# Optimization experiments

Measured on AMD Instinct MI355X. Metric: run time of the kernel, lower is better.

The kernel has to match this reference:

```python
import jax, jax.numpy as jnp
import numpy as np

TMP = 1.0  # temperature from init

def setup_inputs() -> dict:
    key = jax.random.key(0)
    k1, k2, k3 = jax.random.split(key, 3)
    B, D, C = 8192, 1024, 4096
    x = jax.random.normal(k1, (B, D), dtype=jnp.float32)
    mod = jax.random.normal(k2, (B, D), dtype=jnp.float32)
    W = jax.random.normal(k3, (C, D), dtype=jnp.float32) * 0.02  # cls.weight
    return {"x": x, "mod": mod, "W": W}

def reference(x, mod, W):
    # att = softmax(mod / tmp, axis=1) + 1, shape (B, D)
    att = jax.nn.softmax(mod / TMP, axis=1) + 1.0
    # result[b, c] = sum_d W[c, d] * att[b, d] * x[b, d]
    # == (att * x) @ W.T  -- collapses the repeat + per-sample matvec loop
    return jnp.einsum('bd,cd->bc', att * x, W)
```

## Files before the change

kernel.cpp:

```cpp
#include <hip/hip_runtime.h>
#include <hip/hip_bf16.h>
#include <cstdint>
#include <cstddef>

typedef __bf16 bf16_t;
typedef __bf16 bf16x8 __attribute__((ext_vector_type(8)));
typedef __bf16 bf16x4 __attribute__((ext_vector_type(4)));
typedef float  f32x4  __attribute__((ext_vector_type(4)));

#define KDIM 1024
#define NT   16

__global__ void att_scale_kernel(const float* __restrict__ x,
                                 const float* __restrict__ mod,
                                 bf16_t* __restrict__ a, int D) {
  const int b = blockIdx.x;
  const int t = threadIdx.x;
  const size_t row = (size_t)b * D;

  float4 mv = ((const float4*)(mod + row))[t];
  float mx = fmaxf(fmaxf(mv.x, mv.y), fmaxf(mv.z, mv.w));
#pragma unroll
  for (int o = 32; o > 0; o >>= 1) mx = fmaxf(mx, __shfl_xor(mx, o));

  __shared__ float redmax[4];
  __shared__ float redsum[4];
  const int wave = t >> 6, lane = t & 63;
  if (lane == 0) redmax[wave] = mx;
  __syncthreads();
  mx = fmaxf(fmaxf(redmax[0], redmax[1]), fmaxf(redmax[2], redmax[3]));

  float4 e;
  e.x = __expf(mv.x - mx); e.y = __expf(mv.y - mx);
  e.z = __expf(mv.z - mx); e.w = __expf(mv.w - mx);
  float s = (e.x + e.y) + (e.z + e.w);
#pragma unroll
  for (int o = 32; o > 0; o >>= 1) s += __shfl_xor(s, o);
  if (lane == 0) redsum[wave] = s;
  __syncthreads();
  s = (redsum[0] + redsum[1]) + (redsum[2] + redsum[3]);

  const float inv = 1.0f / s;
  float4 xv = ((const float4*)(x + row))[t];
  bf16x4 o4;
  o4[0] = (bf16_t)((e.x * inv + 1.0f) * xv.x);
  o4[1] = (bf16_t)((e.y * inv + 1.0f) * xv.y);
  o4[2] = (bf16_t)((e.z * inv + 1.0f) * xv.z);
  o4[3] = (bf16_t)((e.w * inv + 1.0f) * xv.w);
  *((bf16x4*)(a + row) + t) = o4;
}

__global__ void cast_w_kernel(const float* __restrict__ W,
                              bf16_t* __restrict__ Wb) {
  const size_t i = ((size_t)blockIdx.x * blockDim.x + threadIdx.x) * 8;
  float4 u = *(const float4*)(W + i);
  float4 v = *(const float4*)(W + i + 4);
  bf16x8 o;
  o[0] = (bf16_t)u.x; o[1] = (bf16_t)u.y; o[2] = (bf16_t)u.z; o[3] = (bf16_t)u.w;
  o[4] = (bf16_t)v.x; o[5] = (bf16_t)v.y; o[6] = (bf16_t)v.z; o[7] = (bf16_t)v.w;
  *(bf16x8*)(Wb + i) = o;
}

__global__ __launch_bounds__(512, 2) void gemm256_kernel(
    const bf16_t* __restrict__ A, const bf16_t* __restrict__ B,
    float* __restrict__ C, int M, int N) {
  __shared__ __align__(16) bf16_t lds[2 * 32768];

  const int tid  = threadIdx.x;
  const int wave = tid >> 6;
  const int lane = tid & 63;
  const int quad = lane >> 4;
  const int l16  = lane & 15;
  const int wm   = wave >> 2;
  const int wn   = wave & 3;

  const int nwg = gridDim.x;
  int flat = blockIdx.x;
  flat = (flat & 7) * (nwg >> 3) + (flat >> 3);
  const int ntiles = N >> 8;
  const int m0 = (flat / ntiles) << 8;
  const int n0 = (flat % ntiles) << 8;

  const int trow = tid >> 3;
  const int colg = (tid & 7) ^ (trow & 7);
  const bf16_t* aSrc = A + (size_t)(m0 + trow) * KDIM + colg * 8;
  const bf16_t* bSrc = B + (size_t)(n0 + trow) * KDIM + colg * 8;
  const int ldsW = wave * 512;

#define GLDS(src_, dst_) __builtin_amdgcn_global_load_lds( \
      (const __attribute__((address_space(1))) void*)(src_), \
      (__attribute__((address_space(3))) void*)(dst_), 16, 0, 0)

#define ISSUE_A(h, u_) do { \
      const bf16_t* s_ = aSrc + (size_t)((h) * 128) * KDIM + (u_) * 64; \
      bf16_t* d_ = lds + ((u_) & 1) * 32768 + (h) * 8192 + ldsW; \
      GLDS(s_, d_); \
      GLDS(s_ + (size_t)64 * KDIM, d_ + 4096); \
    } while (0)

#define ISSUE_B(h, u_) do { \
      const bf16_t* s_ = bSrc + (size_t)((h) * 128) * KDIM + (u_) * 64; \
      bf16_t* d_ = lds + ((u_) & 1) * 32768 + 16384 + (h) * 8192 + ldsW; \
      GLDS(s_, d_); \
      GLDS(s_ + (size_t)64 * KDIM, d_ + 4096); \
    } while (0)

  ISSUE_A(0, 0); ISSUE_A(1, 0);
  ISSUE_B(0, 0); ISSUE_B(1, 0);
  ISSUE_B(0, 1); ISSUE_B(1, 1);

  f32x4 acc[8][4];
#pragma unroll
  for (int i = 0; i < 8; ++i)
#pragma unroll
    for (int j = 0; j < 4; ++j) acc[i][j] = (f32x4){0.f, 0.f, 0.f, 0.f};

  const int aBase = (wm * 128 + l16) * 64;
  const int bBase = (wn * 64 + l16) * 64;
  const int c0 = ((quad)     ^ (l16 & 7)) * 8;
  const int c1 = ((4 + quad) ^ (l16 & 7)) * 8;

  asm volatile("s_waitcnt vmcnt(4)" ::: "memory");
  __builtin_amdgcn_s_barrier();

  bf16x8 bfr[4][2];

#define PHASE(q_, ISSUE_STMT, WAIT_STMT) do { \
      bf16x8 af[2][2]; \
      _Pragma("unroll") \
      for (int i = 0; i < 2; ++i) { \
        af[i][0] = *(const bf16x8*)(At + aBase + ((q_) * 32 + i * 16) * 64 + c0); \
        af[i][1] = *(const bf16x8*)(At + aBase + ((q_) * 32 + i * 16) * 64 + c1); \
      } \
      ISSUE_STMT; \
      asm volatile("" ::: "memory"); \
      __builtin_amdgcn_s_barrier(); \
      asm volatile("s_waitcnt lgkmcnt(0)" ::: "memory"); \
      __builtin_amdgcn_s_setprio(1); \
      _Pragma("unroll") \
      for (int i = 0; i < 2; ++i) \
        _Pragma("unroll") \
        for (int j = 0; j < 4; ++j) { \
          acc[(q_) * 2 + i][j] = __builtin_amdgcn_mfma_f32_16x16x32_bf16( \
              af[i][0], bfr[j][0], acc[(q_) * 2 + i][j], 0, 0, 0); \
          acc[(q_) * 2 + i][j] = __builtin_amdgcn_mfma_f32_16x16x32_bf16( \
              af[i][1], bfr[j][1], acc[(q_) * 2 + i][j], 0, 0, 0); \
        } \
      __builtin_amdgcn_s_setprio(0); \
      WAIT_STMT; \
      asm volatile("" ::: "memory"); \
      __builtin_amdgcn_s_barrier(); \
    } while (0)

#pragma unroll 1
  for (int u = 0; u < NT; ++u) {
    const bf16_t* At = lds + (u & 1) * 32768;
    const bf16_t* Bt = At + 16384;

#pragma unroll
    for (int j = 0; j < 4; ++j) {
      bfr[j][0] = *(const bf16x8*)(Bt + bBase + j * 16 * 64 + c0);
      bfr[j][1] = *(const bf16x8*)(Bt + bBase + j * 16 * 64 + c1);
    }
    PHASE(0, if (u + 1 < NT) ISSUE_A(0, u + 1), (void)0);
    PHASE(1, if (u + 1 < NT) ISSUE_A(1, u + 1), (void)0);
    PHASE(2, if (u + 2 < NT) ISSUE_B(0, u + 2), (void)0);
    PHASE(3, if (u + 2 < NT) ISSUE_B(1, u + 2),
          if (u < NT - 2) { asm volatile("s_waitcnt vmcnt(4)" ::: "memory"); }
          else            { asm volatile("s_waitcnt vmcnt(0)" ::: "memory"); });
  }

#pragma unroll
  for (int ri = 0; ri < 8; ++ri) {
    const int mg = m0 + wm * 128 + ri * 16 + quad * 4;
#pragma unroll
    for (int j = 0; j < 4; ++j) {
      const int ng = n0 + wn * 64 + j * 16 + l16;
#pragma unroll
      for (int r = 0; r < 4; ++r)
        C[(size_t)(mg + r) * N + ng] = acc[ri][j][r];
    }
  }
}

extern "C" void kernel_launch(void* const* d_in, const int* in_sizes, int n_in,
                              void* d_out, int out_size, void* d_ws, size_t ws_size,
                              hipStream_t stream) {
  const float* x   = (const float*)d_in[0];
  const float* mod = (const float*)d_in[1];
  const float* W   = (const float*)d_in[2];
  float* out = (float*)d_out;

  const int D = 1024;
  const int Bn = in_sizes[0] / D;
  const int Cn = in_sizes[2] / D;

  bf16_t* a  = (bf16_t*)d_ws;
  bf16_t* Wb = (bf16_t*)((char*)d_ws + (size_t)Bn * D * sizeof(bf16_t));

  att_scale_kernel<<<Bn, 256, 0, stream>>>(x, mod, a, D);
  cast_w_kernel<<<((size_t)Cn * D) / (256 * 8), 256, 0, stream>>>(W, Wb);

  const int nwg = (Bn / 256) * (Cn / 256);
  gemm256_kernel<<<nwg, 512, 0, stream>>>(a, Wb, out, Bn, Cn);
}
```

Measured before the change: 257.0 us.

## Fuse prep kernels and make each GEMM block process two M tiles continuously

Merges the softmax-scale and W-cast kernels into one launch. Each GEMM workgroup now computes two consecutive 256-row M tiles against the same N tile, running one continuous 32-step pipeline that flushes and resets the accumulators halfway. This removes a kernel launch, halves the GEMM grid so each block covers more work, and keeps the prefetch pipeline running across the tile boundary. The cost is half as many workgroups, which on a 256-CU device may lower occupancy and leave load imbalanced, plus a mid-loop store burst.

Result: slower. 272.9 us (+6.2%).

```diff
diff --git a/kernel.cpp b/kernel.cpp
--- a/kernel.cpp
+++ b/kernel.cpp
@@ -10,10 +10,25 @@
 
 #define KDIM 1024
 #define NT   16
-
-__global__ void att_scale_kernel(const float* __restrict__ x,
-                                 const float* __restrict__ mod,
-                                 bf16_t* __restrict__ a, int D) {
+#define NTT  32
+
+__global__ void prep_kernel(const float* __restrict__ x,
+                            const float* __restrict__ mod,
+                            const float* __restrict__ W,
+                            bf16_t* __restrict__ a,
+                            bf16_t* __restrict__ Wb,
+                            int D, int Bn) {
+  if ((int)blockIdx.x >= Bn) {
+    const size_t i = (((size_t)blockIdx.x - Bn) * blockDim.x + threadIdx.x) * 8;
+    float4 u = *(const float4*)(W + i);
+    float4 v = *(const float4*)(W + i + 4);
+    bf16x8 o;
+    o[0] = (bf16_t)u.x; o[1] = (bf16_t)u.y; o[2] = (bf16_t)u.z; o[3] = (bf16_t)u.w;
+    o[4] = (bf16_t)v.x; o[5] = (bf16_t)v.y; o[6] = (bf16_t)v.z; o[7] = (bf16_t)v.w;
+    *(bf16x8*)(Wb + i) = o;
+    return;
+  }
+
   const int b = blockIdx.x;
   const int t = threadIdx.x;
   const size_t row = (size_t)b * D;
@@ -50,17 +65,6 @@
   *((bf16x4*)(a + row) + t) = o4;
 }
 
-__global__ void cast_w_kernel(const float* __restrict__ W,
-                              bf16_t* __restrict__ Wb) {
-  const size_t i = ((size_t)blockIdx.x * blockDim.x + threadIdx.x) * 8;
-  float4 u = *(const float4*)(W + i);
-  float4 v = *(const float4*)(W + i + 4);
-  bf16x8 o;
-  o[0] = (bf16_t)u.x; o[1] = (bf16_t)u.y; o[2] = (bf16_t)u.z; o[3] = (bf16_t)u.w;
-  o[4] = (bf16_t)v.x; o[5] = (bf16_t)v.y; o[6] = (bf16_t)v.z; o[7] = (bf16_t)v.w;
-  *(bf16x8*)(Wb + i) = o;
-}
-
 __global__ __launch_bounds__(512, 2) void gemm256_kernel(
     const bf16_t* __restrict__ A, const bf16_t* __restrict__ B,
     float* __restrict__ C, int M, int N) {
@@ -77,9 +81,9 @@
   const int nwg = gridDim.x;
   int flat = blockIdx.x;
   flat = (flat & 7) * (nwg >> 3) + (flat >> 3);
-  const int ntiles = N >> 8;
-  const int m0 = (flat / ntiles) << 8;
-  const int n0 = (flat % ntiles) << 8;
+  const int mpairs = M >> 9;
+  const int m0 = (flat % mpairs) << 9;
+  const int n0 = (flat / mpairs) << 8;
 
   const int trow = tid >> 3;
   const int colg = (tid & 7) ^ (trow & 7);
@@ -91,16 +95,16 @@
       (const __attribute__((address_space(1))) void*)(src_), \
       (__attribute__((address_space(3))) void*)(dst_), 16, 0, 0)
 
-#define ISSUE_A(h, u_) do { \
-      const bf16_t* s_ = aSrc + (size_t)((h) * 128) * KDIM + (u_) * 64; \
-      bf16_t* d_ = lds + ((u_) & 1) * 32768 + (h) * 8192 + ldsW; \
+#define ISSUE_A(h, t_) do { \
+      const bf16_t* s_ = aSrc + (size_t)((((t_) >> 4) * 256) + (h) * 128) * KDIM + ((t_) & 15) * 64; \
+      bf16_t* d_ = lds + ((t_) & 1) * 32768 + (h) * 8192 + ldsW; \
       GLDS(s_, d_); \
       GLDS(s_ + (size_t)64 * KDIM, d_ + 4096); \
     } while (0)
 
-#define ISSUE_B(h, u_) do { \
-      const bf16_t* s_ = bSrc + (size_t)((h) * 128) * KDIM + (u_) * 64; \
-      bf16_t* d_ = lds + ((u_) & 1) * 32768 + 16384 + (h) * 8192 + ldsW; \
+#define ISSUE_B(h, t_) do { \
+      const bf16_t* s_ = bSrc + (size_t)((h) * 128) * KDIM + ((t_) & 15) * 64; \
+      bf16_t* d_ = lds + ((t_) & 1) * 32768 + 16384 + (h) * 8192 + ldsW; \
       GLDS(s_, d_); \
       GLDS(s_ + (size_t)64 * KDIM, d_ + 4096); \
     } while (0)
@@ -152,9 +156,23 @@
       __builtin_amdgcn_s_barrier(); \
     } while (0)
 
+#define FLUSH(mrep_) do { \
+      _Pragma("unroll") \
+      for (int ri = 0; ri < 8; ++ri) { \
+        const int mg = m0 + (mrep_) * 256 + wm * 128 + ri * 16 + quad * 4; \
+        _Pragma("unroll") \
+        for (int j = 0; j < 4; ++j) { \
+          const int ng = n0 + wn * 64 + j * 16 + l16; \
+          _Pragma("unroll") \
+          for (int r = 0; r < 4; ++r) \
+            C[(size_t)(mg + r) * N + ng] = acc[ri][j][r]; \
+        } \
+      } \
+    } while (0)
+
 #pragma unroll 1
-  for (int u = 0; u < NT; ++u) {
-    const bf16_t* At = lds + (u & 1) * 32768;
+  for (int t = 0; t < NTT; ++t) {
+    const bf16_t* At = lds + (t & 1) * 32768;
     const bf16_t* Bt = At + 16384;
 
 #pragma unroll
@@ -162,25 +180,23 @@
       bfr[j][0] = *(const bf16x8*)(Bt + bBase + j * 16 * 64 + c0);
       bfr[j][1] = *(const bf16x8*)(Bt + bBase + j * 16 * 64 + c1);
     }
-    PHASE(0, if (u + 1 < NT) ISSUE_A(0, u + 1), (void)0);
-    PHASE(1, if (u + 1 < NT) ISSUE_A(1, u + 1), (void)0);
-    PHASE(2, if (u + 2 < NT) ISSUE_B(0, u + 2), (void)0);
-    PHASE(3, if (u + 2 < NT) ISSUE_B(1, u + 2),
-          if (u < NT - 2) { asm volatile("s_waitcnt vmcnt(4)" ::: "memory"); }
-          else            { asm volatile("s_waitcnt vmcnt(0)" ::: "memory"); });
-  }
-
-#pragma unroll
-  for (int ri = 0; ri < 8; ++ri) {
-    const int mg = m0 + wm * 128 + ri * 16 + quad * 4;
-#pragma unroll
-    for (int j = 0; j < 4; ++j) {
-      const int ng = n0 + wn * 64 + j * 16 + l16;
-#pragma unroll
-      for (int r = 0; r < 4; ++r)
-        C[(size_t)(mg + r) * N + ng] = acc[ri][j][r];
+    PHASE(0, if (t + 1 < NTT) ISSUE_A(0, t + 1), (void)0);
+    PHASE(1, if (t + 1 < NTT) ISSUE_A(1, t + 1), (void)0);
+    PHASE(2, if (t + 2 < NTT) ISSUE_B(0, t + 2), (void)0);
+    PHASE(3, if (t + 2 < NTT) ISSUE_B(1, t + 2),
+          if (t < NTT - 2) { asm volatile("s_waitcnt vmcnt(4)" ::: "memory"); }
+          else             { asm volatile("s_waitcnt vmcnt(0)" ::: "memory"); });
+
+    if (t == NT - 1) {
+      FLUSH(0);
+#pragma unroll
+      for (int i = 0; i < 8; ++i)
+#pragma unroll
+        for (int j = 0; j < 4; ++j) acc[i][j] = (f32x4){0.f, 0.f, 0.f, 0.f};
     }
   }
+
+  FLUSH(1);
 }
 
 extern "C" void kernel_launch(void* const* d_in, const int* in_sizes, int n_in,
@@ -198,9 +214,9 @@
   bf16_t* a  = (bf16_t*)d_ws;
   bf16_t* Wb = (bf16_t*)((char*)d_ws + (size_t)Bn * D * sizeof(bf16_t));
 
-  att_scale_kernel<<<Bn, 256, 0, stream>>>(x, mod, a, D);
-  cast_w_kernel<<<((size_t)Cn * D) / (256 * 8), 256, 0, stream>>>(W, Wb);
-
-  const int nwg = (Bn / 256) * (Cn / 256);
+  const int castBlocks = (Cn * D) / (256 * 8);
+  prep_kernel<<<Bn + castBlocks, 256, 0, stream>>>(x, mod, W, a, Wb, D, Bn);
+
+  const int nwg = (Bn / 512) * (Cn / 256);
   gemm256_kernel<<<nwg, 512, 0, stream>>>(a, Wb, out, Bn, Cn);
 }
```
